# Optimization experiments

Measured on AMD Instinct MI355X. Metric: run time of the kernel, lower is better.

Reference implementation:

```python
import jax, jax.numpy as jnp
import numpy as np

E = 23   # unique experts
K = 3    # active experts per token

def setup_inputs() -> dict:
    key = jax.random.key(0)
    ks = jax.random.split(key, 11)
    d, h, B, N = 1024, 768, 16, 196
    s = 0.02  # init scale so sigmoid gate is non-saturated
    return {
        "x":      jax.random.normal(ks[0], (B, N, d), jnp.float32),
        "gate_w": jax.random.normal(ks[1], (d, E), jnp.float32) * s,
        "gate_b": jnp.zeros((E,), jnp.float32),
        "w1":     jax.random.normal(ks[2], (E, d, h), jnp.float32) * s,
        "b1":     jnp.zeros((E, h), jnp.float32),
        "w2":     jax.random.normal(ks[3], (E, h, d), jnp.float32) * s,
        "b2":     jnp.zeros((E, d), jnp.float32),
        "ws1":    jax.random.normal(ks[4], (d, h), jnp.float32) * s,
        "bs1":    jnp.zeros((h,), jnp.float32),
        "ws2":    jax.random.normal(ks[5], (h, d), jnp.float32) * s,
        "bs2":    jnp.zeros((d,), jnp.float32),
    }

def reference(x, gate_w, gate_b, w1, b1, w2, b2, ws1, bs1, ws2, bs2):
    o_shape = x.shape
    xt = x.reshape(-1, o_shape[-1])            # [T, d]
    T = xt.shape[0]

    # gating: sigmoid gate, top-3 (the 'bias' buffer in the source is zeros)
    gw = jax.nn.sigmoid(xt @ gate_w + gate_b)  # [T, E]
    top_vals, top_idx = jax.lax.top_k(gw, K)   # [T, K]
    tw = top_vals / top_vals.sum(-1, keepdims=True)

    # dense combine weights: tw scattered to [T, E] (0 for unselected experts)
    w_dense = jnp.zeros_like(gw).at[jnp.arange(T)[:, None], top_idx].add(tw)

    # expert MLPs (dense-masked equivalent of the grouped dispatch)
    hh = jax.nn.gelu(jnp.einsum('td,edh->teh', xt, w1) + b1, approximate=False)
    eo = jnp.einsum('teh,ehd->ted', hh, w2) + b2          # [T, E, d]

    # shared expert
    shared = jax.nn.gelu(xt @ ws1 + bs1, approximate=False) @ ws2 + bs2

    out = shared + jnp.einsum('ted,te->td', eo, w_dense)  # [T, d]

    # aux load-balancing loss
    gwn = gw / gw.sum(-1, keepdims=True)
    P = gwn.mean(0)                                       # [E]
    counts = jnp.zeros((E,), gw.dtype).at[top_idx.reshape(-1)].add(1.0)
    Fv = E * counts / (K * T)
    aux = (P * Fv).sum()

    return out.reshape(o_shape), aux
```

## Files before the change

kernel.cpp:

```cpp
#include <hip/hip_runtime.h>
#include <hip/hip_bf16.h>

#define T_TOK 3136
#define DDIM  1024
#define HDIM  768
#define NEXP  23
#define TOPK  3
#define MTILE 128
#define NTILE 128
#define KTILE 32
#define LDSB  40
#define MAXTILES 128
#define MAX_SLOTS 16384
#define GATE_BLOCKS 1568
#define XCVT_BLOCKS 3136

typedef __attribute__((ext_vector_type(8))) short  short8;
typedef __attribute__((ext_vector_type(4))) short  short4v;
typedef __attribute__((ext_vector_type(4))) float  floatx4;

__device__ __forceinline__ short f2b(float f) {
    union { float f; unsigned u; } v; v.f = f;
    unsigned r = v.u + 0x7FFFu + ((v.u >> 16) & 1u);
    return (short)(r >> 16);
}
__device__ __forceinline__ float b2f(short s) {
    union { unsigned u; float f; } v; v.u = ((unsigned)(unsigned short)s) << 16; return v.f;
}
__device__ __forceinline__ float gelu_exact(float v) {
    return 0.5f * v * (1.0f + erff(v * 0.70710678118654752f));
}
__device__ __forceinline__ void gld16(const short* g, short* l) {
    __builtin_amdgcn_global_load_lds(
        (const __attribute__((address_space(1))) void*)g,
        (__attribute__((address_space(3))) void*)l, 16, 0, 0);
}
__device__ __forceinline__ void bar_cnt4() {
    asm volatile("s_waitcnt vmcnt(4) lgkmcnt(0)" ::: "memory");
    __builtin_amdgcn_s_barrier();
    __builtin_amdgcn_sched_barrier(0);
}
__device__ __forceinline__ void bar_cnt0() {
    asm volatile("s_waitcnt vmcnt(0) lgkmcnt(0)" ::: "memory");
    __builtin_amdgcn_s_barrier();
    __builtin_amdgcn_sched_barrier(0);
}

__global__ __launch_bounds__(256) void prep_kernel(
    const float* __restrict__ x, short* __restrict__ xb,
    const float* __restrict__ gw, float* __restrict__ gwT, float* __restrict__ Pf)
{
    __shared__ float tile[32][33];
    if (blockIdx.x < XCVT_BLOCKS) {
        if (blockIdx.x == 0 && threadIdx.x < NEXP) Pf[threadIdx.x] = 0.f;
        int i = blockIdx.x * 256 + threadIdx.x;
        float4 v = ((const float4*)x)[i];
        short4v s = { f2b(v.x), f2b(v.y), f2b(v.z), f2b(v.w) };
        ((short4v*)xb)[i] = s;
        return;
    }
    const int kt = blockIdx.x - XCVT_BLOCKS;
    const int tx = threadIdx.x & 31, ty = threadIdx.x >> 5;
    #pragma unroll
    for (int i = 0; i < 4; i++) {
        int k = ty + i * 8;
        tile[k][tx] = (tx < NEXP) ? gw[(size_t)(kt * 32 + k) * NEXP + tx] : 0.f;
    }
    __syncthreads();
    #pragma unroll
    for (int i = 0; i < 4; i++) {
        int e = ty + i * 8;
        if (e < 24) gwT[(size_t)e * DDIM + kt * 32 + tx] = tile[tx][e];
    }
}

__global__ __launch_bounds__(256) void gate_kernel(
    const float* __restrict__ x, const float* __restrict__ gwT, const float* __restrict__ gb,
    float* __restrict__ Pf, int* __restrict__ top_idx, float* __restrict__ top_w)
{
    const int tid = threadIdx.x;
    const int lane = tid & 63, wave = tid >> 6;
    const int ebase = wave * 6;
    __shared__ float sg[24];
    __shared__ float accP[NEXP];
    if (tid < NEXP) accP[tid] = 0.f;

    for (int t = blockIdx.x; t < T_TOK; t += GATE_BLOCKS) {
        const float4* xr4 = (const float4*)(x + (size_t)t * DDIM);
        float4 xv[4];
        #pragma unroll
        for (int j = 0; j < 4; j++) xv[j] = xr4[j * 64 + lane];

        double a0 = 0, a1 = 0, a2 = 0, a3 = 0, a4 = 0, a5 = 0;
        #pragma unroll
        for (int j = 0; j < 4; j++) {
            const float4* gp = (const float4*)gwT + (size_t)ebase * 256 + j * 64 + lane;
            float4 g0 = gp[0 * 256], g1 = gp[1 * 256], g2 = gp[2 * 256];
            float4 g3 = gp[3 * 256], g4 = gp[4 * 256], g5 = gp[5 * 256];
            float4 xj = xv[j];
            a0 += (double)xj.x * g0.x + (double)xj.y * g0.y + (double)xj.z * g0.z + (double)xj.w * g0.w;
            a1 += (double)xj.x * g1.x + (double)xj.y * g1.y + (double)xj.z * g1.z + (double)xj.w * g1.w;
            a2 += (double)xj.x * g2.x + (double)xj.y * g2.y + (double)xj.z * g2.z + (double)xj.w * g2.w;
            a3 += (double)xj.x * g3.x + (double)xj.y * g3.y + (double)xj.z * g3.z + (double)xj.w * g3.w;
            a4 += (double)xj.x * g4.x + (double)xj.y * g4.y + (double)xj.z * g4.z + (double)xj.w * g4.w;
            a5 += (double)xj.x * g5.x + (double)xj.y * g5.y + (double)xj.z * g5.z + (double)xj.w * g5.w;
        }
        #pragma unroll
        for (int off = 32; off > 0; off >>= 1) {
            a0 += __shfl_xor(a0, off);
            a1 += __shfl_xor(a1, off);
            a2 += __shfl_xor(a2, off);
            a3 += __shfl_xor(a3, off);
            a4 += __shfl_xor(a4, off);
            a5 += __shfl_xor(a5, off);
        }

        if (lane == 0) {
            double av[6] = { a0, a1, a2, a3, a4, a5 };
            #pragma unroll
            for (int i = 0; i < 6; i++) {
                int e = ebase + i;
                if (e < NEXP) {
                    float z = (float)av[i] + gb[e];
                    sg[e] = 1.0f / (1.0f + expf(-z));
                }
            }
        }
        __syncthreads();

        if (tid < NEXP) {
            float s = 0.f;
            #pragma unroll
            for (int e = 0; e < NEXP; e++) s += sg[e];
            accP[tid] += sg[tid] / s;
        }
        if (tid == 0) {
            float v0 = -1.f, v1 = -1.f, v2 = -1.f; int i0 = 0, i1 = 0, i2 = 0;
            for (int e = 0; e < NEXP; e++) {
                float v = sg[e];
                if (v > v0)      { v2 = v1; i2 = i1; v1 = v0; i1 = i0; v0 = v; i0 = e; }
                else if (v > v1) { v2 = v1; i2 = i1; v1 = v; i1 = e; }
                else if (v > v2) { v2 = v; i2 = e; }
            }
            float ts = v0 + v1 + v2;
            top_idx[t * 3 + 0] = i0; top_w[t * 3 + 0] = v0 / ts;
            top_idx[t * 3 + 1] = i1; top_w[t * 3 + 1] = v1 / ts;
            top_idx[t * 3 + 2] = i2; top_w[t * 3 + 2] = v2 / ts;
        }
        __syncthreads();
    }
    if (tid < NEXP) atomicAdd(&Pf[tid], accP[tid]);
}

__global__ __launch_bounds__(1024) void route_kernel(
    const int* __restrict__ top_idx, const float* __restrict__ Pf,
    int* __restrict__ ntl,
    int* __restrict__ slot_t, int* __restrict__ slot_of,
    int* __restrict__ tmap_e, int* __restrict__ tmap_b,
    float* __restrict__ out_aux)
{
    __shared__ int h[NEXP];
    __shared__ int lfill[NEXP];
    __shared__ int soffs[NEXP + 1];
    __shared__ int sntl[NEXP + 1];
    const int tid = threadIdx.x;
    if (tid < NEXP) { h[tid] = 0; lfill[tid] = 0; }
    __syncthreads();
    for (int i = tid; i < T_TOK * 3; i += 1024) atomicAdd(&h[top_idx[i]], 1);
    __syncthreads();
    if (tid == 0) {
        int o = 0, ti = 0;
        for (int e = 0; e < NEXP; e++) {
            int c = h[e];
            int nt = (c + MTILE - 1) / MTILE;
            soffs[e] = o; sntl[e] = nt; ntl[e] = nt;
            for (int j = 0; j < nt; j++) { tmap_e[ti] = e; tmap_b[ti] = o + j * MTILE; ti++; }
            o += nt * MTILE;
        }
        int nts = (T_TOK + MTILE - 1) / MTILE;
        soffs[NEXP] = o; sntl[NEXP] = nts; ntl[NEXP] = nts;
        for (int j = 0; j < nts; j++) { tmap_e[ti] = NEXP; tmap_b[ti] = o + j * MTILE; ti++; }
        ntl[NEXP + 1] = ti;
        float aux = 0.f;
        for (int e = 0; e < NEXP; e++) {
            float P = Pf[e] / (float)T_TOK;
            float F = (float)NEXP * (float)h[e] / (float)(TOPK * T_TOK);
            aux += P * F;
        }
        out_aux[0] = aux;
    }
    __syncthreads();
    for (int e = 0; e <= NEXP; e++) {
        int cnt = (e < NEXP) ? h[e] : T_TOK;
        int s0 = soffs[e] + cnt, s1 = soffs[e] + sntl[e] * MTILE;
        for (int s = s0 + tid; s < s1; s += 1024) slot_t[s] = 0;
    }
    for (int t = tid; t < T_TOK; t += 1024) {
        #pragma unroll
        for (int k = 0; k < TOPK; k++) {
            int e = top_idx[t * 3 + k];
            int pos = atomicAdd(&lfill[e], 1);
            int s = soffs[e] + pos;
            slot_t[s] = t;
            slot_of[t * 4 + k] = s;
        }
        int s = soffs[NEXP] + t;
        slot_t[s] = t;
        slot_of[t * 4 + 3] = s;
    }
}

__global__ __launch_bounds__(512) void gemm1_kernel(
    const short* __restrict__ xb,
    const float* __restrict__ w1, const float* __restrict__ b1,
    const float* __restrict__ ws1, const float* __restrict__ bs1,
    const int* __restrict__ tmap_e, const int* __restrict__ tmap_b,
    const int* __restrict__ ntl,
    const int* __restrict__ slot_t, short* __restrict__ hh)
{
    const int L = blockIdx.x;
    const int xcd = L & 7, sl = L >> 3;
    const int ty = xcd * 16 + sl / 6, tx = sl % 6;
    if (ty >= ntl[NEXP + 1]) return;
    const int e = tmap_e[ty];
    const int slot_base = tmap_b[ty];
    const int n0 = tx * NTILE;
    const float* __restrict__ Wf = (e < NEXP) ? (w1 + (size_t)e * DDIM * HDIM) : ws1;
    const float* __restrict__ Bv = (e < NEXP) ? (b1 + (size_t)e * HDIM) : bs1;

    __shared__ __align__(16) short As[2][MTILE * KTILE];
    __shared__ __align__(16) short Bs[2][NTILE * LDSB];
    __shared__ int toks[MTILE];

    const int tid = threadIdx.x;
    for (int i = tid; i < MTILE; i += 512) toks[i] = slot_t[slot_base + i];

    const int lane = tid & 63, wave = tid >> 6;
    const int mbase = (wave & 1) * 64, nbase = (wave >> 1) * 32;
    const int lc = lane & 15, q = lane >> 4;
    const int xq8 = (q ^ ((lc >> 1) & 3)) << 3;

    const int srow = wave * 16 + (lane >> 2);
    const int c8   = (lane & 3) * 8;

    __syncthreads();
    const short* gA = xb + (size_t)toks[srow] * DDIM + c8;
    const int lofs = wave * 512;

    const int cn = lane;
    const float* gW = Wf + (size_t)(4 * wave) * HDIM + n0 + 2 * cn;
    const int bws = ((((wave >> 1) ^ (cn & 3)) << 3) + (wave & 1) * 4);
    const int bofs0 = (2 * cn) * LDSB + bws, bofs1 = (2 * cn + 1) * LDSB + bws;

    floatx4 acc[4][2];
    #pragma unroll
    for (int m = 0; m < 4; m++)
        #pragma unroll
        for (int n = 0; n < 2; n++) acc[m][n] = (floatx4)0.f;

    const int NT = DDIM / KTILE;
    float2 f[4];
    #pragma unroll
    for (int j = 0; j < 4; j++) f[j] = *(const float2*)(gW + (size_t)j * HDIM);
    gld16(gA, &As[0][lofs]);
    __builtin_amdgcn_sched_barrier(0);
    {
        short4v s0, s1;
        #pragma unroll
        for (int j = 0; j < 4; j++) { s0[j] = f2b(f[j].x); s1[j] = f2b(f[j].y); }
        *(short4v*)&Bs[0][bofs0] = s0;
        *(short4v*)&Bs[0][bofs1] = s1;
    }
    #pragma unroll
    for (int j = 0; j < 4; j++) f[j] = *(const float2*)(gW + (size_t)(KTILE + j) * HDIM);
    bar_cnt4();

    for (int t = 0; t < NT; t++) {
        const int cur = t & 1;
        if (t + 1 < NT) {
            gld16(gA + (t + 1) * KTILE, &As[cur ^ 1][lofs]);
            __builtin_amdgcn_sched_barrier(0);
            short4v s0, s1;
            #pragma unroll
            for (int j = 0; j < 4; j++) { s0[j] = f2b(f[j].x); s1[j] = f2b(f[j].y); }
            *(short4v*)&Bs[cur ^ 1][bofs0] = s0;
            *(short4v*)&Bs[cur ^ 1][bofs1] = s1;
        }
        if (t + 2 < NT) {
            #pragma unroll
            for (int j = 0; j < 4; j++)
                f[j] = *(const float2*)(gW + (size_t)((t + 2) * KTILE + j) * HDIM);
        }
        short8 af[4], bf[2];
        #pragma unroll
        for (int m = 0; m < 4; m++) af[m] = *(const short8*)&As[cur][(mbase + m * 16 + lc) * KTILE + q * 8];
        #pragma unroll
        for (int n = 0; n < 2; n++) bf[n] = *(const short8*)&Bs[cur][(nbase + n * 16 + lc) * LDSB + xq8];
        #pragma unroll
        for (int m = 0; m < 4; m++)
            #pragma unroll
            for (int n = 0; n < 2; n++)
                acc[m][n] = __builtin_amdgcn_mfma_f32_16x16x32_bf16(af[m], bf[n], acc[m][n], 0, 0, 0);
        if (t + 1 < NT) {
            if (t + 2 < NT) bar_cnt4();
            else            bar_cnt0();
        }
    }

    #pragma unroll
    for (int n = 0; n < 2; n++) {
        const int col = n0 + nbase + n * 16 + lc;
        const float bb = Bv[col];
        #pragma unroll
        for (int m = 0; m < 4; m++) {
            const int rbase = slot_base + mbase + m * 16 + q * 4;
            #pragma unroll
            for (int r = 0; r < 4; r++) {
                float v = acc[m][n][r] + bb;
                hh[(size_t)(rbase + r) * HDIM + col] = f2b(gelu_exact(v));
            }
        }
    }
}

__global__ __launch_bounds__(512) void gemm2_kernel(
    const short* __restrict__ hh,
    const float* __restrict__ w2, const float* __restrict__ b2,
    const float* __restrict__ ws2, const float* __restrict__ bs2,
    const int* __restrict__ tmap_e, const int* __restrict__ tmap_b,
    const int* __restrict__ ntl,
    short* __restrict__ eo)
{
    const int L = blockIdx.x;
    const int xcd = L & 7, sl = L >> 3;
    const int ty = xcd * 16 + sl / 8, tx = sl & 7;
    if (ty >= ntl[NEXP + 1]) return;
    const int e = tmap_e[ty];
    const int slot_base = tmap_b[ty];
    const int n0 = tx * NTILE;
    const float* __restrict__ Wf = (e < NEXP) ? (w2 + (size_t)e * HDIM * DDIM) : ws2;
    const float* __restrict__ Bv = (e < NEXP) ? (b2 + (size_t)e * DDIM) : bs2;

    __shared__ __align__(16) short As[2][MTILE * KTILE];
    __shared__ __align__(16) short Bs[2][NTILE * LDSB];

    const int tid = threadIdx.x;
    const int lane = tid & 63, wave = tid >> 6;
    const int mbase = (wave & 1) * 64, nbase = (wave >> 1) * 32;
    const int lc = lane & 15, q = lane >> 4;
    const int xq8 = (q ^ ((lc >> 1) & 3)) << 3;

    const int srow = wave * 16 + (lane >> 2);
    const int c8   = (lane & 3) * 8;

    const short* gA = hh + (size_t)(slot_base + srow) * HDIM + c8;
    const int lofs = wave * 512;

    const int cn = lane;
    const float* gW = Wf + (size_t)(4 * wave) * DDIM + n0 + 2 * cn;
    const int bws = ((((wave >> 1) ^ (cn & 3)) << 3) + (wave & 1) * 4);
    const int bofs0 = (2 * cn) * LDSB + bws, bofs1 = (2 * cn + 1) * LDSB + bws;

    floatx4 acc[4][2];
    #pragma unroll
    for (int m = 0; m < 4; m++)
        #pragma unroll
        for (int n = 0; n < 2; n++) acc[m][n] = (floatx4)0.f;

    const int NT = HDIM / KTILE;
    float2 f[4];
    #pragma unroll
    for (int j = 0; j < 4; j++) f[j] = *(const float2*)(gW + (size_t)j * DDIM);
    gld16(gA, &As[0][lofs]);
    __builtin_amdgcn_sched_barrier(0);
    {
        short4v s0, s1;
        #pragma unroll
        for (int j = 0; j < 4; j++) { s0[j] = f2b(f[j].x); s1[j] = f2b(f[j].y); }
        *(short4v*)&Bs[0][bofs0] = s0;
        *(short4v*)&Bs[0][bofs1] = s1;
    }
    #pragma unroll
    for (int j = 0; j < 4; j++) f[j] = *(const float2*)(gW + (size_t)(KTILE + j) * DDIM);
    bar_cnt4();

    for (int t = 0; t < NT; t++) {
        const int cur = t & 1;
        if (t + 1 < NT) {
            gld16(gA + (t + 1) * KTILE, &As[cur ^ 1][lofs]);
            __builtin_amdgcn_sched_barrier(0);
            short4v s0, s1;
            #pragma unroll
            for (int j = 0; j < 4; j++) { s0[j] = f2b(f[j].x); s1[j] = f2b(f[j].y); }
            *(short4v*)&Bs[cur ^ 1][bofs0] = s0;
            *(short4v*)&Bs[cur ^ 1][bofs1] = s1;
        }
        if (t + 2 < NT) {
            #pragma unroll
            for (int j = 0; j < 4; j++)
                f[j] = *(const float2*)(gW + (size_t)((t + 2) * KTILE + j) * DDIM);
        }
        short8 af[4], bf[2];
        #pragma unroll
        for (int m = 0; m < 4; m++) af[m] = *(const short8*)&As[cur][(mbase + m * 16 + lc) * KTILE + q * 8];
        #pragma unroll
        for (int n = 0; n < 2; n++) bf[n] = *(const short8*)&Bs[cur][(nbase + n * 16 + lc) * LDSB + xq8];
        #pragma unroll
        for (int m = 0; m < 4; m++)
            #pragma unroll
            for (int n = 0; n < 2; n++)
                acc[m][n] = __builtin_amdgcn_mfma_f32_16x16x32_bf16(af[m], bf[n], acc[m][n], 0, 0, 0);
        if (t + 1 < NT) {
            if (t + 2 < NT) bar_cnt4();
            else            bar_cnt0();
        }
    }

    #pragma unroll
    for (int n = 0; n < 2; n++) {
        const int col = n0 + nbase + n * 16 + lc;
        const float bb = Bv[col];
        #pragma unroll
        for (int m = 0; m < 4; m++) {
            const int rbase = slot_base + mbase + m * 16 + q * 4;
            #pragma unroll
            for (int r = 0; r < 4; r++)
                eo[(size_t)(rbase + r) * DDIM + col] = f2b(acc[m][n][r] + bb);
        }
    }
}

__global__ __launch_bounds__(256) void combine_kernel(
    const short* __restrict__ eo, const float* __restrict__ top_w,
    const int* __restrict__ slot_of, float* __restrict__ out)
{
    const int t = blockIdx.x;
    const int c = threadIdx.x * 4;
    const int s0 = slot_of[t * 4 + 0], s1 = slot_of[t * 4 + 1];
    const int s2 = slot_of[t * 4 + 2], s3 = slot_of[t * 4 + 3];
    const float w0 = top_w[t * 3 + 0], w1 = top_w[t * 3 + 1], w2 = top_w[t * 3 + 2];
    short4v a = *(const short4v*)(eo + (size_t)s0 * DDIM + c);
    short4v b = *(const short4v*)(eo + (size_t)s1 * DDIM + c);
    short4v d = *(const short4v*)(eo + (size_t)s2 * DDIM + c);
    short4v s = *(const short4v*)(eo + (size_t)s3 * DDIM + c);
    float4 o;
    o.x = b2f(s.x) + w0 * b2f(a.x) + w1 * b2f(b.x) + w2 * b2f(d.x);
    o.y = b2f(s.y) + w0 * b2f(a.y) + w1 * b2f(b.y) + w2 * b2f(d.y);
    o.z = b2f(s.z) + w0 * b2f(a.z) + w1 * b2f(b.z) + w2 * b2f(d.z);
    o.w = b2f(s.w) + w0 * b2f(a.w) + w1 * b2f(b.w) + w2 * b2f(d.w);
    *(float4*)(out + (size_t)t * DDIM + c) = o;
}

extern "C" void kernel_launch(void* const* d_in, const int* in_sizes, int n_in,
                              void* d_out, int out_size, void* d_ws, size_t ws_size,
                              hipStream_t stream)
{
    const float* x   = (const float*)d_in[0];
    const float* gw  = (const float*)d_in[1];
    const float* gb  = (const float*)d_in[2];
    const float* w1  = (const float*)d_in[3];
    const float* b1  = (const float*)d_in[4];
    const float* w2  = (const float*)d_in[5];
    const float* b2  = (const float*)d_in[6];
    const float* ws1 = (const float*)d_in[7];
    const float* bs1 = (const float*)d_in[8];
    const float* ws2 = (const float*)d_in[9];
    const float* bs2 = (const float*)d_in[10];
    float* out = (float*)d_out;

    char* p = (char*)d_ws;
    auto alloc = [&](size_t bytes) -> char* {
        char* r = p; p += (bytes + 255) & ~(size_t)255; return r;
    };
    int*   top_idx  = (int*)  alloc((size_t)T_TOK * 3 * 4);
    float* top_w    = (float*)alloc((size_t)T_TOK * 3 * 4);
    float* Pf       = (float*)alloc(NEXP * 4);
    int*   ntl      = (int*)  alloc((NEXP + 2) * 4);
    int*   slot_t   = (int*)  alloc((size_t)MAX_SLOTS * 4);
    int*   slot_of  = (int*)  alloc((size_t)T_TOK * 4 * 4);
    int*   tmap_e   = (int*)  alloc((size_t)MAXTILES * 4);
    int*   tmap_b   = (int*)  alloc((size_t)MAXTILES * 4);
    float* gwT      = (float*)alloc((size_t)24 * DDIM * 4);
    short* xb       = (short*)alloc((size_t)T_TOK * DDIM * 2);
    short* hh       = (short*)alloc((size_t)MAX_SLOTS * HDIM * 2);
    short* eo       = (short*)alloc((size_t)MAX_SLOTS * DDIM * 2);

    prep_kernel<<<XCVT_BLOCKS + DDIM / 32, 256, 0, stream>>>(x, xb, gw, gwT, Pf);
    gate_kernel<<<GATE_BLOCKS, 256, 0, stream>>>(x, gwT, gb, Pf, top_idx, top_w);
    route_kernel<<<1, 1024, 0, stream>>>(top_idx, Pf, ntl, slot_t, slot_of,
                                         tmap_e, tmap_b, out + (size_t)T_TOK * DDIM);
    gemm1_kernel<<<8 * 16 * 6, 512, 0, stream>>>(
        xb, w1, b1, ws1, bs1, tmap_e, tmap_b, ntl, slot_t, hh);
    gemm2_kernel<<<8 * 16 * 8, 512, 0, stream>>>(
        hh, w2, b2, ws2, bs2, tmap_e, tmap_b, ntl, eo);
    combine_kernel<<<T_TOK, 256, 0, stream>>>(eo, top_w, slot_of, out);
}
```

Before: 376.5 us.

## Double the M tile to 256 rows with 64x64 per-wave tiles in expert GEMMs

Both grouped GEMM kernels now process 256 token rows per block instead of 128. Each of the 8 waves computes a 64x64 output sub-tile with 16 accumulators instead of 64x32 with 8. Each converted fp32-to-bf16 weight tile is therefore reused across twice as many rows, which cuts the weight reads and conversion work per FLOP. The tile map capacity, slot buffer size and grid sizes are adjusted to match. The cost is higher register pressure, more padding waste per expert, and fewer blocks to spread across the CUs.

```diff
diff --git a/kernel.cpp b/kernel.cpp
--- a/kernel.cpp
+++ b/kernel.cpp
@@ -6,12 +6,12 @@
 #define HDIM  768
 #define NEXP  23
 #define TOPK  3
-#define MTILE 128
+#define MTILE 256
 #define NTILE 128
 #define KTILE 32
 #define LDSB  40
-#define MAXTILES 128
-#define MAX_SLOTS 16384
+#define TYCAP 80
+#define MAX_SLOTS 20480
 #define GATE_BLOCKS 1568
 #define XCVT_BLOCKS 3136
 
@@ -220,7 +220,7 @@
 {
     const int L = blockIdx.x;
     const int xcd = L & 7, sl = L >> 3;
-    const int ty = xcd * 16 + sl / 6, tx = sl % 6;
+    const int ty = xcd * 10 + sl / 6, tx = sl % 6;
     if (ty >= ntl[NEXP + 1]) return;
     const int e = tmap_e[ty];
     const int slot_base = tmap_b[ty];
@@ -236,7 +236,7 @@
     for (int i = tid; i < MTILE; i += 512) toks[i] = slot_t[slot_base + i];
 
     const int lane = tid & 63, wave = tid >> 6;
-    const int mbase = (wave & 1) * 64, nbase = (wave >> 1) * 32;
+    const int mbase = (wave & 3) * 64, nbase = (wave >> 2) * 64;
     const int lc = lane & 15, q = lane >> 4;
     const int xq8 = (q ^ ((lc >> 1) & 3)) << 3;
 
@@ -244,25 +244,27 @@
     const int c8   = (lane & 3) * 8;
 
     __syncthreads();
-    const short* gA = xb + (size_t)toks[srow] * DDIM + c8;
-    const int lofs = wave * 512;
+    const short* gA0 = xb + (size_t)toks[srow]       * DDIM + c8;
+    const short* gA1 = xb + (size_t)toks[128 + srow] * DDIM + c8;
+    const int lofs0 = wave * 512, lofs1 = 4096 + wave * 512;
 
     const int cn = lane;
     const float* gW = Wf + (size_t)(4 * wave) * HDIM + n0 + 2 * cn;
     const int bws = ((((wave >> 1) ^ (cn & 3)) << 3) + (wave & 1) * 4);
     const int bofs0 = (2 * cn) * LDSB + bws, bofs1 = (2 * cn + 1) * LDSB + bws;
 
-    floatx4 acc[4][2];
+    floatx4 acc[4][4];
     #pragma unroll
     for (int m = 0; m < 4; m++)
         #pragma unroll
-        for (int n = 0; n < 2; n++) acc[m][n] = (floatx4)0.f;
+        for (int n = 0; n < 4; n++) acc[m][n] = (floatx4)0.f;
 
     const int NT = DDIM / KTILE;
     float2 f[4];
     #pragma unroll
     for (int j = 0; j < 4; j++) f[j] = *(const float2*)(gW + (size_t)j * HDIM);
-    gld16(gA, &As[0][lofs]);
+    gld16(gA0, &As[0][lofs0]);
+    gld16(gA1, &As[0][lofs1]);
     __builtin_amdgcn_sched_barrier(0);
     {
         short4v s0, s1;
@@ -278,7 +280,8 @@
     for (int t = 0; t < NT; t++) {
         const int cur = t & 1;
         if (t + 1 < NT) {
-            gld16(gA + (t + 1) * KTILE, &As[cur ^ 1][lofs]);
+            gld16(gA0 + (t + 1) * KTILE, &As[cur ^ 1][lofs0]);
+            gld16(gA1 + (t + 1) * KTILE, &As[cur ^ 1][lofs1]);
             __builtin_amdgcn_sched_barrier(0);
             short4v s0, s1;
             #pragma unroll
@@ -291,15 +294,15 @@
             for (int j = 0; j < 4; j++)
                 f[j] = *(const float2*)(gW + (size_t)((t + 2) * KTILE + j) * HDIM);
         }
-        short8 af[4], bf[2];
+        short8 af[4], bf[4];
         #pragma unroll
         for (int m = 0; m < 4; m++) af[m] = *(const short8*)&As[cur][(mbase + m * 16 + lc) * KTILE + q * 8];
         #pragma unroll
-        for (int n = 0; n < 2; n++) bf[n] = *(const short8*)&Bs[cur][(nbase + n * 16 + lc) * LDSB + xq8];
+        for (int n = 0; n < 4; n++) bf[n] = *(const short8*)&Bs[cur][(nbase + n * 16 + lc) * LDSB + xq8];
         #pragma unroll
         for (int m = 0; m < 4; m++)
             #pragma unroll
-            for (int n = 0; n < 2; n++)
+            for (int n = 0; n < 4; n++)
                 acc[m][n] = __builtin_amdgcn_mfma_f32_16x16x32_bf16(af[m], bf[n], acc[m][n], 0, 0, 0);
         if (t + 1 < NT) {
             if (t + 2 < NT) bar_cnt4();
@@ -308,7 +311,7 @@
     }
 
     #pragma unroll
-    for (int n = 0; n < 2; n++) {
+    for (int n = 0; n < 4; n++) {
         const int col = n0 + nbase + n * 16 + lc;
         const float bb = Bv[col];
         #pragma unroll
@@ -333,7 +336,7 @@
 {
     const int L = blockIdx.x;
     const int xcd = L & 7, sl = L >> 3;
-    const int ty = xcd * 16 + sl / 8, tx = sl & 7;
+    const int ty = xcd * 10 + (sl >> 3), tx = sl & 7;
     if (ty >= ntl[NEXP + 1]) return;
     const int e = tmap_e[ty];
     const int slot_base = tmap_b[ty];
@@ -346,32 +349,34 @@
 
     const int tid = threadIdx.x;
     const int lane = tid & 63, wave = tid >> 6;
-    const int mbase = (wave & 1) * 64, nbase = (wave >> 1) * 32;
+    const int mbase = (wave & 3) * 64, nbase = (wave >> 2) * 64;
     const int lc = lane & 15, q = lane >> 4;
     const int xq8 = (q ^ ((lc >> 1) & 3)) << 3;
 
     const int srow = wave * 16 + (lane >> 2);
     const int c8   = (lane & 3) * 8;
 
-    const short* gA = hh + (size_t)(slot_base + srow) * HDIM + c8;
-    const int lofs = wave * 512;
+    const short* gA0 = hh + (size_t)(slot_base + srow)       * HDIM + c8;
+    const short* gA1 = hh + (size_t)(slot_base + 128 + srow) * HDIM + c8;
+    const int lofs0 = wave * 512, lofs1 = 4096 + wave * 512;
 
     const int cn = lane;
     const float* gW = Wf + (size_t)(4 * wave) * DDIM + n0 + 2 * cn;
     const int bws = ((((wave >> 1) ^ (cn & 3)) << 3) + (wave & 1) * 4);
     const int bofs0 = (2 * cn) * LDSB + bws, bofs1 = (2 * cn + 1) * LDSB + bws;
 
-    floatx4 acc[4][2];
+    floatx4 acc[4][4];
     #pragma unroll
     for (int m = 0; m < 4; m++)
         #pragma unroll
-        for (int n = 0; n < 2; n++) acc[m][n] = (floatx4)0.f;
+        for (int n = 0; n < 4; n++) acc[m][n] = (floatx4)0.f;
 
     const int NT = HDIM / KTILE;
     float2 f[4];
     #pragma unroll
     for (int j = 0; j < 4; j++) f[j] = *(const float2*)(gW + (size_t)j * DDIM);
-    gld16(gA, &As[0][lofs]);
+    gld16(gA0, &As[0][lofs0]);
+    gld16(gA1, &As[0][lofs1]);
     __builtin_amdgcn_sched_barrier(0);
     {
         short4v s0, s1;
@@ -387,7 +392,8 @@
     for (int t = 0; t < NT; t++) {
         const int cur = t & 1;
         if (t + 1 < NT) {
-            gld16(gA + (t + 1) * KTILE, &As[cur ^ 1][lofs]);
+            gld16(gA0 + (t + 1) * KTILE, &As[cur ^ 1][lofs0]);
+            gld16(gA1 + (t + 1) * KTILE, &As[cur ^ 1][lofs1]);
             __builtin_amdgcn_sched_barrier(0);
             short4v s0, s1;
             #pragma unroll
@@ -400,15 +406,15 @@
             for (int j = 0; j < 4; j++)
                 f[j] = *(const float2*)(gW + (size_t)((t + 2) * KTILE + j) * DDIM);
         }
-        short8 af[4], bf[2];
+        short8 af[4], bf[4];
         #pragma unroll
         for (int m = 0; m < 4; m++) af[m] = *(const short8*)&As[cur][(mbase + m * 16 + lc) * KTILE + q * 8];
         #pragma unroll
-        for (int n = 0; n < 2; n++) bf[n] = *(const short8*)&Bs[cur][(nbase + n * 16 + lc) * LDSB + xq8];
+        for (int n = 0; n < 4; n++) bf[n] = *(const short8*)&Bs[cur][(nbase + n * 16 + lc) * LDSB + xq8];
         #pragma unroll
         for (int m = 0; m < 4; m++)
             #pragma unroll
-            for (int n = 0; n < 2; n++)
+            for (int n = 0; n < 4; n++)
                 acc[m][n] = __builtin_amdgcn_mfma_f32_16x16x32_bf16(af[m], bf[n], acc[m][n], 0, 0, 0);
         if (t + 1 < NT) {
             if (t + 2 < NT) bar_cnt4();
@@ -417,7 +423,7 @@
     }
 
     #pragma unroll
-    for (int n = 0; n < 2; n++) {
+    for (int n = 0; n < 4; n++) {
         const int col = n0 + nbase + n * 16 + lc;
         const float bb = Bv[col];
         #pragma unroll
@@ -478,8 +484,8 @@
     int*   ntl      = (int*)  alloc((NEXP + 2) * 4);
     int*   slot_t   = (int*)  alloc((size_t)MAX_SLOTS * 4);
     int*   slot_of  = (int*)  alloc((size_t)T_TOK * 4 * 4);
-    int*   tmap_e   = (int*)  alloc((size_t)MAXTILES * 4);
-    int*   tmap_b   = (int*)  alloc((size_t)MAXTILES * 4);
+    int*   tmap_e   = (int*)  alloc((size_t)TYCAP * 4);
+    int*   tmap_b   = (int*)  alloc((size_t)TYCAP * 4);
     float* gwT      = (float*)alloc((size_t)24 * DDIM * 4);
     short* xb       = (short*)alloc((size_t)T_TOK * DDIM * 2);
     short* hh       = (short*)alloc((size_t)MAX_SLOTS * HDIM * 2);
@@ -489,9 +495,9 @@
     gate_kernel<<<GATE_BLOCKS, 256, 0, stream>>>(x, gwT, gb, Pf, top_idx, top_w);
     route_kernel<<<1, 1024, 0, stream>>>(top_idx, Pf, ntl, slot_t, slot_of,
                                          tmap_e, tmap_b, out + (size_t)T_TOK * DDIM);
-    gemm1_kernel<<<8 * 16 * 6, 512, 0, stream>>>(
+    gemm1_kernel<<<8 * 10 * 6, 512, 0, stream>>>(
         xb, w1, b1, ws1, bs1, tmap_e, tmap_b, ntl, slot_t, hh);
-    gemm2_kernel<<<8 * 16 * 8, 512, 0, stream>>>(
+    gemm2_kernel<<<8 * 10 * 8, 512, 0, stream>>>(
         hh, w2, b2, ws2, bs2, tmap_e, tmap_b, ntl, eo);
     combine_kernel<<<T_TOK, 256, 0, stream>>>(eo, top_w, slot_of, out);
 }
```

Result: slower. 391.4 us (+4.0%).
